# Kernel optimization log

Hardware: AMD Instinct MI355X
Metric: run time of the kernel (lower is better)

The kernel has to match this reference:

```python
import jax, jax.numpy as jnp
import numpy as np

DIM = 1024
MULT = 4
HID = DIM * MULT
E = 8
B, S = 2, 2048


def _rmsnorm(x):
    # zeta SimpleRMSNorm: F.normalize(x, dim=-1) * sqrt(dim)
    n = jnp.linalg.norm(x, axis=-1, keepdims=True)
    return x / jnp.maximum(n, 1e-12) * jnp.sqrt(jnp.asarray(x.shape[-1], x.dtype))


def _act_quant(x):
    # per-token 8-bit absmax quant (BitNet b1.58), straight-through in fwd math
    scale = 127.0 / jnp.clip(jnp.max(jnp.abs(x), axis=-1, keepdims=True), 1e-5)
    q = jnp.clip(jnp.round(x * scale), -128, 127) / scale
    return x + jax.lax.stop_gradient(q - x)


def _w_quant(w, axes):
    # ternary weight quant with per-matrix mean-abs scale
    scale = 1.0 / jnp.clip(jnp.mean(jnp.abs(w), axis=axes, keepdims=True), 1e-5)
    q = jnp.clip(jnp.round(w * scale), -1, 1) / scale
    return w + jax.lax.stop_gradient(q - w)


def setup_inputs() -> dict:
    key = jax.random.key(0)
    ks = jax.random.split(key, 8)
    sd = 0.02
    x = jax.random.normal(ks[0], (B, S, DIM), dtype=jnp.float32)
    gw = jax.random.normal(ks[1], (E, DIM), dtype=jnp.float32) * sd
    gb = jnp.zeros((E,), dtype=jnp.float32)
    w1 = jax.random.normal(ks[2], (E, HID, DIM), dtype=jnp.float32) * sd
    b1 = jnp.zeros((E, HID), dtype=jnp.float32)
    w2 = jax.random.normal(ks[3], (E, DIM, HID), dtype=jnp.float32) * sd
    b2 = jnp.zeros((E, DIM), dtype=jnp.float32)
    return {"x": x, "gw": gw, "gb": gb, "w1": w1, "b1": b1, "w2": w2, "b2": b2}


def reference(x, gw, gb, w1, b1, w2, b2):
    # BitLinear input preprocessing: RMSNorm then 8-bit activation quant
    xq = _act_quant(_rmsnorm(x))  # [B,S,D]

    # Gate: softmax(BitLinear(dim, E))
    logits = jnp.einsum("bsd,ed->bse", xq, _w_quant(gw, axes=(0, 1))) + gb
    gates = jax.nn.softmax(logits, axis=-1)  # [B,S,E]

    # Experts: BitLinear -> GELU -> BitLinear, quant scales per expert
    w1q = _w_quant(w1, axes=(1, 2))  # [E,H,D]
    w2q = _w_quant(w2, axes=(1, 2))  # [E,D,H]
    h = jnp.einsum("bsd,ehd->bseh", xq, w1q) + b1  # [B,S,E,H]
    a = jax.nn.gelu(h, approximate=False)
    aq = _act_quant(_rmsnorm(a))
    expert_out = jnp.einsum("bseh,edh->bsed", aq, w2q) + b2  # [B,S,E,D]

    # softmax-weighted sum over experts
    return jnp.einsum("bse,bsed->bsd", gates, expert_out)
```

## Files before the change

### kernel.cpp

```cpp
#include <hip/hip_runtime.h>


#define T_TOK 4096
#define DIMS  1024
#define HID   4096
#define NE    8
#define ROWB  8192ull

typedef __attribute__((ext_vector_type(4))) int       i32x4;
typedef __attribute__((ext_vector_type(8))) _Float16  f16x8;
typedef __attribute__((ext_vector_type(4))) _Float16  f16x4;

__device__ __forceinline__ float block_sum(float v, float* buf, int tid) {
  #pragma unroll
  for (int o = 32; o > 0; o >>= 1) v += __shfl_down(v, o, 64);
  __syncthreads();
  if ((tid & 63) == 0) buf[tid >> 6] = v;
  __syncthreads();
  return buf[0] + buf[1] + buf[2] + buf[3];
}
__device__ __forceinline__ float block_max(float v, float* buf, int tid) {
  #pragma unroll
  for (int o = 32; o > 0; o >>= 1) { float t = __shfl_down(v, o, 64); v = fmaxf(v, t); }
  __syncthreads();
  if ((tid & 63) == 0) buf[tid >> 6] = v;
  __syncthreads();
  return fmaxf(fmaxf(buf[0], buf[1]), fmaxf(buf[2], buf[3]));
}

__device__ __forceinline__ void gl_lds16(const void* g, void* l) {
  __builtin_amdgcn_global_load_lds(
      (const __attribute__((address_space(1))) unsigned int*)g,
      (__attribute__((address_space(3))) unsigned int*)l, 16, 0, 0);
}

__device__ __forceinline__ int q8(float v) {
  return ((int)fminf(fmaxf(rintf(v), -128.0f), 127.0f)) & 0xff;
}

__global__ __launch_bounds__(256) void wabs_sum_kernel(
    const float4* __restrict__ w, int n_f4, int shift, float* __restrict__ sums) {
  __shared__ float buf[4];
  const int tid = threadIdx.x;
  const int base = blockIdx.x * 4096;
  float acc = 0.0f;
  for (int k = 0; k < 16; ++k) {
    int fi = base + k * 256 + tid;
    if (fi < n_f4) {
      float4 v = w[fi];
      acc += fabsf(v.x) + fabsf(v.y) + fabsf(v.z) + fabsf(v.w);
    }
  }
  acc = block_sum(acc, buf, tid);
  if (tid == 0) atomicAdd(&sums[base >> shift], acc);
}

__global__ void mkscales_kernel(const float* __restrict__ wsum, float* __restrict__ sc) {
  if (threadIdx.x == 0) {
    #pragma unroll
    for (int e = 0; e < NE; ++e) {
      float m1 = fmaxf(wsum[e] * (1.0f / 4194304.0f), 1e-5f);
      sc[e] = m1; sc[8 + e] = 1.0f / m1;
      float m2 = fmaxf(wsum[8 + e] * (1.0f / 4194304.0f), 1e-5f);
      sc[16 + e] = m2; sc[24 + e] = 1.0f / m2;
    }
    float mg = fmaxf(wsum[16] * (1.0f / 8192.0f), 1e-5f);
    sc[32] = mg; sc[33] = 1.0f / mg;
  }
}

__global__ __launch_bounds__(256) void wquant_kernel(
    const float4* __restrict__ w, int* __restrict__ o, int n_f4, int shift,
    const float* __restrict__ qs) {
  int fi = blockIdx.x * 256 + threadIdx.x;
  if (fi >= n_f4) return;
  const float s = qs[fi >> shift];
  float4 v = w[fi];
  int b0 = ((int)fminf(fmaxf(rintf(v.x * s), -1.0f), 1.0f)) & 0xff;
  int b1 = ((int)fminf(fmaxf(rintf(v.y * s), -1.0f), 1.0f)) & 0xff;
  int b2 = ((int)fminf(fmaxf(rintf(v.z * s), -1.0f), 1.0f)) & 0xff;
  int b3 = ((int)fminf(fmaxf(rintf(v.w * s), -1.0f), 1.0f)) & 0xff;
  o[fi] = b0 | (b1 << 8) | (b2 << 16) | (b3 << 24);
}

__global__ __launch_bounds__(256) void preprocess_kernel(
    const float* __restrict__ x, const float* __restrict__ gw,
    const float* __restrict__ gb, const float* __restrict__ scales,
    int* __restrict__ qx, float* __restrict__ inv_sx, float* __restrict__ gates) {
  __shared__ float buf[4];
  const int t = blockIdx.x, tid = threadIdx.x;
  const float4 xv = ((const float4*)(x + (size_t)t * DIMS))[tid];
  float ss = xv.x * xv.x + xv.y * xv.y + xv.z * xv.z + xv.w * xv.w;
  ss = block_sum(ss, buf, tid);
  const float rr = 32.0f / fmaxf(sqrtf(ss), 1e-12f);
  const float y0 = xv.x * rr, y1 = xv.y * rr, y2 = xv.z * rr, y3 = xv.w * rr;
  float am = fmaxf(fmaxf(fabsf(y0), fabsf(y1)), fmaxf(fabsf(y2), fabsf(y3)));
  am = block_max(am, buf, tid);
  const float aclip = fmaxf(am, 1e-5f);
  const float qsc = 127.0f / aclip;
  const float q0 = fminf(fmaxf(rintf(y0 * qsc), -128.0f), 127.0f);
  const float q1 = fminf(fmaxf(rintf(y1 * qsc), -128.0f), 127.0f);
  const float q2 = fminf(fmaxf(rintf(y2 * qsc), -128.0f), 127.0f);
  const float q3 = fminf(fmaxf(rintf(y3 * qsc), -128.0f), 127.0f);
  qx[t * 256 + tid] = (((int)q0) & 0xff) | ((((int)q1) & 0xff) << 8) |
                      ((((int)q2) & 0xff) << 16) | ((((int)q3) & 0xff) << 24);

  const float gsabs = scales[32], gqs = scales[33];
  float lg[NE];
  #pragma unroll
  for (int e = 0; e < NE; ++e) {
    const float4 gv = ((const float4*)(gw + e * DIMS))[tid];
    float t0 = fminf(fmaxf(rintf(gv.x * gqs), -1.0f), 1.0f);
    float t1 = fminf(fmaxf(rintf(gv.y * gqs), -1.0f), 1.0f);
    float t2 = fminf(fmaxf(rintf(gv.z * gqs), -1.0f), 1.0f);
    float t3 = fminf(fmaxf(rintf(gv.w * gqs), -1.0f), 1.0f);
    lg[e] = q0 * t0 + q1 * t1 + q2 * t2 + q3 * t3;
  }
  #pragma unroll
  for (int e = 0; e < NE; ++e) lg[e] = block_sum(lg[e], buf, tid);
  if (tid == 0) {
    const float isx = aclip / 127.0f;
    inv_sx[t] = isx;
    float l[NE], mx = -1e30f;
    #pragma unroll
    for (int e = 0; e < NE; ++e) { l[e] = lg[e] * (isx * gsabs) + gb[e]; mx = fmaxf(mx, l[e]); }
    float s = 0.0f;
    #pragma unroll
    for (int e = 0; e < NE; ++e) { l[e] = expf(l[e] - mx); s += l[e]; }
    const float inv = 1.0f / s;
    #pragma unroll
    for (int e = 0; e < NE; ++e) gates[t * NE + e] = l[e] * inv;
  }
}

__global__ __launch_bounds__(256) void gemm1_kernel(
    const char* __restrict__ qx, const char* __restrict__ w1q,
    const float* __restrict__ scales, const float* __restrict__ inv_sx,
    const float* __restrict__ b1, char* __restrict__ aqa) {
  __shared__ __align__(16) char sA[128 * 64];
  __shared__ __align__(16) char sB[128 * 64];
  const int e = blockIdx.z;
  const char* A = qx;
  const char* Bm = w1q + (size_t)e * HID * DIMS;
  char* obase = aqa + (size_t)e * T_TOK * ROWB;
  const int m0 = blockIdx.x * 128, n0 = blockIdx.y * 128;
  const int tid = threadIdx.x, lane = tid & 63, wv = tid >> 6;
  const int wr = (wv >> 1) * 64, wc = (wv & 1) * 64, lm = lane & 15, lq = lane >> 4;
  i32x4 acc[4][4] = {};
  for (int k0 = 0; k0 < DIMS; k0 += 64) {
    #pragma unroll
    for (int is = 0; is < 2; ++is) {
      const int c = is * 256 + tid;
      const int row = c >> 2, kc = (c & 3) * 16;
      gl_lds16(A + (size_t)(m0 + row) * DIMS + k0 + kc, &sA[c * 16]);
      gl_lds16(Bm + (size_t)(n0 + row) * DIMS + k0 + kc, &sB[c * 16]);
    }
    __syncthreads();
    i32x4 av[4], bv[4];
    #pragma unroll
    for (int i = 0; i < 4; ++i) av[i] = *(const i32x4*)&sA[(wr + i * 16 + lm) * 64 + lq * 16];
    #pragma unroll
    for (int j = 0; j < 4; ++j) bv[j] = *(const i32x4*)&sB[(wc + j * 16 + lm) * 64 + lq * 16];
    #pragma unroll
    for (int i = 0; i < 4; ++i)
      #pragma unroll
      for (int j = 0; j < 4; ++j)
        acc[i][j] = __builtin_amdgcn_mfma_i32_16x16x64_i8(av[i], bv[j], acc[i][j], 0, 0, 0);
    __syncthreads();
  }
  const float s1 = scales[e];
  #pragma unroll
  for (int i = 0; i < 4; ++i) {
    #pragma unroll
    for (int r = 0; r < 4; ++r) {
      const int row = m0 + wr + i * 16 + lq * 4 + r;
      const float rs = inv_sx[row] * s1;
      _Float16* orow = (_Float16*)(obase + (size_t)row * ROWB);
      #pragma unroll
      for (int j = 0; j < 4; ++j) {
        const int col = n0 + wc + j * 16 + lm;
        const float h = (float)acc[i][j][r] * rs + b1[e * HID + col];
        const float a = 0.5f * h * (1.0f + erff(h * 0.70710678118654752f));
        orow[col] = (_Float16)a;
      }
    }
  }
}

__global__ __launch_bounds__(256) void rowquant_kernel(
    char* __restrict__ aqa, float* __restrict__ inv_sa) {
  __shared__ float buf[4];
  const size_t R = blockIdx.x;
  char* rowb = aqa + R * ROWB;
  const int tid = threadIdx.x;
  f16x8 v0 = ((const f16x8*)rowb)[tid * 2];
  f16x8 v1 = ((const f16x8*)rowb)[tid * 2 + 1];
  float f[16];
  #pragma unroll
  for (int k = 0; k < 8; ++k) { f[k] = (float)v0[k]; f[8 + k] = (float)v1[k]; }
  float ss = 0.0f;
  #pragma unroll
  for (int k = 0; k < 16; ++k) ss += f[k] * f[k];
  ss = block_sum(ss, buf, tid);
  const float rr = 64.0f / fmaxf(sqrtf(ss), 1e-12f);
  float am = 0.0f;
  #pragma unroll
  for (int k = 0; k < 16; ++k) am = fmaxf(am, fabsf(f[k] * rr));
  am = block_max(am, buf, tid);
  const float aclip = fmaxf(am, 1e-5f);
  const float qsc = rr * 127.0f / aclip;
  int4 o;
  o.x = q8(f[0] * qsc) | (q8(f[1] * qsc) << 8) | (q8(f[2] * qsc) << 16) | (q8(f[3] * qsc) << 24);
  o.y = q8(f[4] * qsc) | (q8(f[5] * qsc) << 8) | (q8(f[6] * qsc) << 16) | (q8(f[7] * qsc) << 24);
  o.z = q8(f[8] * qsc) | (q8(f[9] * qsc) << 8) | (q8(f[10] * qsc) << 16) | (q8(f[11] * qsc) << 24);
  o.w = q8(f[12] * qsc) | (q8(f[13] * qsc) << 8) | (q8(f[14] * qsc) << 16) | (q8(f[15] * qsc) << 24);
  ((int4*)rowb)[tid] = o;
  if (tid == 0) inv_sa[R] = aclip / 127.0f;
}

__global__ __launch_bounds__(256) void gemm2_kernel(
    const char* __restrict__ aqa, const char* __restrict__ w2q,
    const float* __restrict__ scales, const float* __restrict__ inv_sa,
    const float* __restrict__ b2, const float* __restrict__ gates,
    float* __restrict__ dst, int use_atomic) {
  __shared__ __align__(16) char sA[128 * 64];
  __shared__ __align__(16) char sB[128 * 64];
  const int e = blockIdx.z;
  const char* A = aqa + (size_t)e * T_TOK * ROWB;
  const char* Bm = w2q + (size_t)e * DIMS * HID;
  const int n0 = blockIdx.x * 128, m0 = blockIdx.y * 128;
  const int tid = threadIdx.x, lane = tid & 63, wv = tid >> 6;
  const int wr = (wv >> 1) * 64, wc = (wv & 1) * 64, lm = lane & 15, lq = lane >> 4;
  i32x4 acc[4][4] = {};
  for (int k0 = 0; k0 < HID; k0 += 64) {
    #pragma unroll
    for (int is = 0; is < 2; ++is) {
      const int c = is * 256 + tid;
      const int row = c >> 2, kc = (c & 3) * 16;
      gl_lds16(A + (size_t)(m0 + row) * ROWB + k0 + kc, &sA[c * 16]);
      gl_lds16(Bm + (size_t)(n0 + row) * HID + k0 + kc, &sB[c * 16]);
    }
    __syncthreads();
    i32x4 av[4], bv[4];
    #pragma unroll
    for (int i = 0; i < 4; ++i) av[i] = *(const i32x4*)&sA[(wr + i * 16 + lm) * 64 + lq * 16];
    #pragma unroll
    for (int j = 0; j < 4; ++j) bv[j] = *(const i32x4*)&sB[(wc + j * 16 + lm) * 64 + lq * 16];
    #pragma unroll
    for (int i = 0; i < 4; ++i)
      #pragma unroll
      for (int j = 0; j < 4; ++j)
        acc[i][j] = __builtin_amdgcn_mfma_i32_16x16x64_i8(av[i], bv[j], acc[i][j], 0, 0, 0);
    __syncthreads();
  }
  const float s2 = scales[16 + e];
  #pragma unroll
  for (int i = 0; i < 4; ++i) {
    #pragma unroll
    for (int r = 0; r < 4; ++r) {
      const int row = m0 + wr + i * 16 + lq * 4 + r;
      const float rs = inv_sa[(size_t)e * T_TOK + row] * s2;
      const float g = gates[row * NE + e];
      #pragma unroll
      for (int j = 0; j < 4; ++j) {
        const int col = n0 + wc + j * 16 + lm;
        const float v = g * ((float)acc[i][j][r] * rs + b2[e * DIMS + col]);
        if (use_atomic) atomicAdd(&dst[(size_t)row * DIMS + col], v);
        else dst[((size_t)e * T_TOK + row) * DIMS + col] = v;
      }
    }
  }
}

__global__ __launch_bounds__(256) void reduce_kernel(
    const float4* __restrict__ eout, float4* __restrict__ out) {
  const int i = blockIdx.x * 256 + threadIdx.x;
  float4 s = eout[i];
  #pragma unroll
  for (int e = 1; e < NE; ++e) {
    float4 v = eout[(size_t)e * (T_TOK * DIMS / 4) + i];
    s.x += v.x; s.y += v.y; s.z += v.z; s.w += v.w;
  }
  out[i] = s;
}

extern "C" void kernel_launch(void* const* d_in, const int* in_sizes, int n_in,
                              void* d_out, int out_size, void* d_ws, size_t ws_size,
                              hipStream_t stream) {
  const float* x  = (const float*)d_in[0];
  const float* gw = (const float*)d_in[1];
  const float* gb = (const float*)d_in[2];
  const float* w1 = (const float*)d_in[3];
  const float* b1 = (const float*)d_in[4];
  const float* w2 = (const float*)d_in[5];
  const float* b2 = (const float*)d_in[6];
  float* outp = (float*)d_out;
  char* ws = (char*)d_ws;

  float* wsum   = (float*)(ws + 0);
  float* scales = (float*)(ws + 256);
  float* inv_sx = (float*)(ws + 4096);
  float* gates  = (float*)(ws + 20480);
  float* inv_sa = (float*)(ws + 151552);
  char*  qx     = ws + 282624;
  char*  w1q    = ws + 4476928;
  char*  w2q    = ws + 38031360;
  char*  aqa    = ws + 71585792;
  float* eout   = (float*)(ws + 340021248);

  const bool has_eout = ws_size >= 474238976ull;

  hipMemsetAsync(wsum, 0, 17 * sizeof(float), stream);
  wabs_sum_kernel<<<2048, 256, 0, stream>>>((const float4*)w1, 8388608, 20, wsum + 0);
  wabs_sum_kernel<<<2048, 256, 0, stream>>>((const float4*)w2, 8388608, 20, wsum + 8);
  wabs_sum_kernel<<<1,    256, 0, stream>>>((const float4*)gw, 2048,    30, wsum + 16);
  mkscales_kernel<<<1, 64, 0, stream>>>(wsum, scales);
  wquant_kernel<<<32768, 256, 0, stream>>>((const float4*)w1, (int*)w1q, 8388608, 20, scales + 8);
  wquant_kernel<<<32768, 256, 0, stream>>>((const float4*)w2, (int*)w2q, 8388608, 20, scales + 24);
  preprocess_kernel<<<4096, 256, 0, stream>>>(x, gw, gb, scales, (int*)qx, inv_sx, gates);

  gemm1_kernel<<<dim3(32, 32, 8), 256, 0, stream>>>(qx, w1q, scales, inv_sx, b1, aqa);
  rowquant_kernel<<<32768, 256, 0, stream>>>(aqa, inv_sa);

  if (has_eout) {
    gemm2_kernel<<<dim3(8, 32, 8), 256, 0, stream>>>(
        aqa, w2q, scales, inv_sa, b2, gates, eout, 0);
    reduce_kernel<<<4096, 256, 0, stream>>>((const float4*)eout, (float4*)outp);
  } else {
    hipMemsetAsync(outp, 0, (size_t)out_size * sizeof(float), stream);
    gemm2_kernel<<<dim3(8, 32, 8), 256, 0, stream>>>(
        aqa, w2q, scales, inv_sa, b2, gates, outp, 1);
  }
}
```

Baseline: 1.018 ms.

## Enlarge int8 GEMM tiles to 256x128x128 with XOR-swizzled LDS layout

Both int8 MFMA GEMMs now use 256x128 output tiles with a K step of 128 instead of 128x128x64. Each warp computes 128x64, and LDS chunks are XOR-swizzled by row to avoid bank conflicts on fragment reads. The launch bounds request two blocks per CU. The larger tiles raise arithmetic intensity and halve the number of barrier-synchronised K iterations, at the cost of 48KB of LDS and 128 accumulator registers per thread, which may reduce occupancy or cause spills.

```diff
diff --git a/kernel.cpp b/kernel.cpp
--- a/kernel.cpp
+++ b/kernel.cpp
@@ -9,7 +9,6 @@
 
 typedef __attribute__((ext_vector_type(4))) int       i32x4;
 typedef __attribute__((ext_vector_type(8))) _Float16  f16x8;
-typedef __attribute__((ext_vector_type(4))) _Float16  f16x4;
 
 __device__ __forceinline__ float block_sum(float v, float* buf, int tid) {
   #pragma unroll
@@ -36,6 +35,10 @@
 
 __device__ __forceinline__ int q8(float v) {
   return ((int)fminf(fmaxf(rintf(v), -128.0f), 127.0f)) & 0xff;
+}
+
+__device__ __forceinline__ const i32x4* frag(const char* s, int row, int ckW) {
+  return (const i32x4*)&s[row * 128 + ((ckW ^ (row & 7)) << 4)];
 }
 
 __global__ __launch_bounds__(256) void wabs_sum_kernel(
@@ -133,44 +136,53 @@
   }
 }
 
-__global__ __launch_bounds__(256) void gemm1_kernel(
+__global__ __launch_bounds__(256, 2) void gemm1_kernel(
     const char* __restrict__ qx, const char* __restrict__ w1q,
     const float* __restrict__ scales, const float* __restrict__ inv_sx,
     const float* __restrict__ b1, char* __restrict__ aqa) {
-  __shared__ __align__(16) char sA[128 * 64];
-  __shared__ __align__(16) char sB[128 * 64];
+  __shared__ __align__(16) char sA[256 * 128];
+  __shared__ __align__(16) char sB[128 * 128];
   const int e = blockIdx.z;
   const char* A = qx;
   const char* Bm = w1q + (size_t)e * HID * DIMS;
   char* obase = aqa + (size_t)e * T_TOK * ROWB;
-  const int m0 = blockIdx.x * 128, n0 = blockIdx.y * 128;
+  const int n0 = blockIdx.x * 128, m0 = blockIdx.y * 256;
   const int tid = threadIdx.x, lane = tid & 63, wv = tid >> 6;
-  const int wr = (wv >> 1) * 64, wc = (wv & 1) * 64, lm = lane & 15, lq = lane >> 4;
-  i32x4 acc[4][4] = {};
-  for (int k0 = 0; k0 < DIMS; k0 += 64) {
-    #pragma unroll
-    for (int is = 0; is < 2; ++is) {
-      const int c = is * 256 + tid;
-      const int row = c >> 2, kc = (c & 3) * 16;
-      gl_lds16(A + (size_t)(m0 + row) * DIMS + k0 + kc, &sA[c * 16]);
-      gl_lds16(Bm + (size_t)(n0 + row) * DIMS + k0 + kc, &sB[c * 16]);
+  const int wr = (wv >> 1) * 128, wc = (wv & 1) * 64, lm = lane & 15, lq = lane >> 4;
+  i32x4 acc[8][4] = {};
+  for (int k0 = 0; k0 < DIMS; k0 += 128) {
+    #pragma unroll
+    for (int it = 0; it < 8; ++it) {
+      const int c = it * 256 + tid;
+      const int row = c >> 3, ckG = (c & 7) ^ (row & 7);
+      gl_lds16(A + (size_t)(m0 + row) * DIMS + k0 + ckG * 16, &sA[c * 16]);
+    }
+    #pragma unroll
+    for (int it = 0; it < 4; ++it) {
+      const int c = it * 256 + tid;
+      const int row = c >> 3, ckG = (c & 7) ^ (row & 7);
+      gl_lds16(Bm + (size_t)(n0 + row) * DIMS + k0 + ckG * 16, &sB[c * 16]);
     }
     __syncthreads();
-    i32x4 av[4], bv[4];
-    #pragma unroll
-    for (int i = 0; i < 4; ++i) av[i] = *(const i32x4*)&sA[(wr + i * 16 + lm) * 64 + lq * 16];
-    #pragma unroll
-    for (int j = 0; j < 4; ++j) bv[j] = *(const i32x4*)&sB[(wc + j * 16 + lm) * 64 + lq * 16];
-    #pragma unroll
-    for (int i = 0; i < 4; ++i)
-      #pragma unroll
-      for (int j = 0; j < 4; ++j)
-        acc[i][j] = __builtin_amdgcn_mfma_i32_16x16x64_i8(av[i], bv[j], acc[i][j], 0, 0, 0);
+    #pragma unroll
+    for (int kk = 0; kk < 2; ++kk) {
+      i32x4 av[8], bv[4];
+      const int ckW = kk * 4 + lq;
+      #pragma unroll
+      for (int i = 0; i < 8; ++i) av[i] = *frag(sA, wr + i * 16 + lm, ckW);
+      #pragma unroll
+      for (int j = 0; j < 4; ++j) bv[j] = *frag(sB, wc + j * 16 + lm, ckW);
+      #pragma unroll
+      for (int i = 0; i < 8; ++i)
+        #pragma unroll
+        for (int j = 0; j < 4; ++j)
+          acc[i][j] = __builtin_amdgcn_mfma_i32_16x16x64_i8(av[i], bv[j], acc[i][j], 0, 0, 0);
+    }
     __syncthreads();
   }
   const float s1 = scales[e];
   #pragma unroll
-  for (int i = 0; i < 4; ++i) {
+  for (int i = 0; i < 8; ++i) {
     #pragma unroll
     for (int r = 0; r < 4; ++r) {
       const int row = m0 + wr + i * 16 + lq * 4 + r;
@@ -218,44 +230,53 @@
   if (tid == 0) inv_sa[R] = aclip / 127.0f;
 }
 
-__global__ __launch_bounds__(256) void gemm2_kernel(
+__global__ __launch_bounds__(256, 2) void gemm2_kernel(
     const char* __restrict__ aqa, const char* __restrict__ w2q,
     const float* __restrict__ scales, const float* __restrict__ inv_sa,
     const float* __restrict__ b2, const float* __restrict__ gates,
     float* __restrict__ dst, int use_atomic) {
-  __shared__ __align__(16) char sA[128 * 64];
-  __shared__ __align__(16) char sB[128 * 64];
+  __shared__ __align__(16) char sA[256 * 128];
+  __shared__ __align__(16) char sB[128 * 128];
   const int e = blockIdx.z;
   const char* A = aqa + (size_t)e * T_TOK * ROWB;
   const char* Bm = w2q + (size_t)e * DIMS * HID;
-  const int n0 = blockIdx.x * 128, m0 = blockIdx.y * 128;
+  const int n0 = blockIdx.x * 128, m0 = blockIdx.y * 256;
   const int tid = threadIdx.x, lane = tid & 63, wv = tid >> 6;
-  const int wr = (wv >> 1) * 64, wc = (wv & 1) * 64, lm = lane & 15, lq = lane >> 4;
-  i32x4 acc[4][4] = {};
-  for (int k0 = 0; k0 < HID; k0 += 64) {
-    #pragma unroll
-    for (int is = 0; is < 2; ++is) {
-      const int c = is * 256 + tid;
-      const int row = c >> 2, kc = (c & 3) * 16;
-      gl_lds16(A + (size_t)(m0 + row) * ROWB + k0 + kc, &sA[c * 16]);
-      gl_lds16(Bm + (size_t)(n0 + row) * HID + k0 + kc, &sB[c * 16]);
+  const int wr = (wv >> 1) * 128, wc = (wv & 1) * 64, lm = lane & 15, lq = lane >> 4;
+  i32x4 acc[8][4] = {};
+  for (int k0 = 0; k0 < HID; k0 += 128) {
+    #pragma unroll
+    for (int it = 0; it < 8; ++it) {
+      const int c = it * 256 + tid;
+      const int row = c >> 3, ckG = (c & 7) ^ (row & 7);
+      gl_lds16(A + (size_t)(m0 + row) * ROWB + k0 + ckG * 16, &sA[c * 16]);
+    }
+    #pragma unroll
+    for (int it = 0; it < 4; ++it) {
+      const int c = it * 256 + tid;
+      const int row = c >> 3, ckG = (c & 7) ^ (row & 7);
+      gl_lds16(Bm + (size_t)(n0 + row) * HID + k0 + ckG * 16, &sB[c * 16]);
     }
     __syncthreads();
-    i32x4 av[4], bv[4];
-    #pragma unroll
-    for (int i = 0; i < 4; ++i) av[i] = *(const i32x4*)&sA[(wr + i * 16 + lm) * 64 + lq * 16];
-    #pragma unroll
-    for (int j = 0; j < 4; ++j) bv[j] = *(const i32x4*)&sB[(wc + j * 16 + lm) * 64 + lq * 16];
-    #pragma unroll
-    for (int i = 0; i < 4; ++i)
-      #pragma unroll
-      for (int j = 0; j < 4; ++j)
-        acc[i][j] = __builtin_amdgcn_mfma_i32_16x16x64_i8(av[i], bv[j], acc[i][j], 0, 0, 0);
+    #pragma unroll
+    for (int kk = 0; kk < 2; ++kk) {
+      i32x4 av[8], bv[4];
+      const int ckW = kk * 4 + lq;
+      #pragma unroll
+      for (int i = 0; i < 8; ++i) av[i] = *frag(sA, wr + i * 16 + lm, ckW);
+      #pragma unroll
+      for (int j = 0; j < 4; ++j) bv[j] = *frag(sB, wc + j * 16 + lm, ckW);
+      #pragma unroll
+      for (int i = 0; i < 8; ++i)
+        #pragma unroll
+        for (int j = 0; j < 4; ++j)
+          acc[i][j] = __builtin_amdgcn_mfma_i32_16x16x64_i8(av[i], bv[j], acc[i][j], 0, 0, 0);
+    }
     __syncthreads();
   }
   const float s2 = scales[16 + e];
   #pragma unroll
-  for (int i = 0; i < 4; ++i) {
+  for (int i = 0; i < 8; ++i) {
     #pragma unroll
     for (int r = 0; r < 4; ++r) {
       const int row = m0 + wr + i * 16 + lq * 4 + r;
@@ -319,16 +340,16 @@
   wquant_kernel<<<32768, 256, 0, stream>>>((const float4*)w2, (int*)w2q, 8388608, 20, scales + 24);
   preprocess_kernel<<<4096, 256, 0, stream>>>(x, gw, gb, scales, (int*)qx, inv_sx, gates);
 
-  gemm1_kernel<<<dim3(32, 32, 8), 256, 0, stream>>>(qx, w1q, scales, inv_sx, b1, aqa);
+  gemm1_kernel<<<dim3(32, 16, 8), 256, 0, stream>>>(qx, w1q, scales, inv_sx, b1, aqa);
   rowquant_kernel<<<32768, 256, 0, stream>>>(aqa, inv_sa);
 
   if (has_eout) {
-    gemm2_kernel<<<dim3(8, 32, 8), 256, 0, stream>>>(
+    gemm2_kernel<<<dim3(8, 16, 8), 256, 0, stream>>>(
         aqa, w2q, scales, inv_sa, b2, gates, eout, 0);
     reduce_kernel<<<4096, 256, 0, stream>>>((const float4*)eout, (float4*)outp);
   } else {
     hipMemsetAsync(outp, 0, (size_t)out_size * sizeof(float), stream);
-    gemm2_kernel<<<dim3(8, 32, 8), 256, 0, stream>>>(
+    gemm2_kernel<<<dim3(8, 16, 8), 256, 0, stream>>>(
         aqa, w2q, scales, inv_sa, b2, gates, outp, 1);
   }
 }
```

Result: faster. 939.5 us (-7.7%).
